# Optimization experiments

Measured on AMD Instinct MI355X. Metric: run time of the kernel, lower is better.

Reference implementation:

```python
import jax, jax.numpy as jnp
import numpy as np

B, C_IN, T, N_VERTEX = 2, 64, 12, 2048
KS, C_OUT = 3, 64
NNZ = 98304  # Ks * n_vertex * avg_degree(16)


def setup_inputs() -> dict:
    key = jax.random.key(0)
    k0, k1, k2, k3, k4, k5 = jax.random.split(key, 6)
    x = jax.random.normal(k0, (B, C_IN, T, N_VERTEX), jnp.float32)
    # kaiming-uniform-ish init for weight [Ks, c_in, c_out]
    bound_w = float(np.sqrt(6.0 / C_IN))
    weight = jax.random.uniform(k1, (KS, C_IN, C_OUT), jnp.float32, -bound_w, bound_w)
    bound_b = float(1.0 / np.sqrt(C_OUT))
    bias = jax.random.uniform(k2, (C_OUT,), jnp.float32, -bound_b, bound_b)
    # sparse chebconv_filter in COO: shape [n_vertex, Ks*n_vertex]
    filter_rows = jax.random.randint(k3, (NNZ,), 0, N_VERTEX)
    filter_cols = jax.random.randint(k4, (NNZ,), 0, KS * N_VERTEX)
    filter_vals = jax.random.normal(k5, (NNZ,), jnp.float32) * 0.1
    return dict(x=x, weight=weight, bias=bias, filter_vals=filter_vals,
                filter_rows=filter_rows, filter_cols=filter_cols)


def reference(x, weight, bias, filter_vals, filter_rows, filter_cols):
    b, c_in, t, n = x.shape
    ks, _, c_out = weight.shape
    # dense GEMM: [B*T*n (row-major flatten of B,c_in,T,n keeping last dim c_in), c_in] @ [c_in, Ks*c_out]
    xw = x.reshape(-1, c_in) @ weight.reshape(c_in, ks * c_out)  # [B*c_in*T*n/c_in, Ks*c_out]
    xw = xw.reshape(n * ks, -1)                                  # [n*Ks, B*T*c_out]
    # spmm with COO filter [n, n*Ks]: gather columns, scale, scatter-add to rows
    gathered = filter_vals[:, None] * xw[filter_cols]            # [nnz, B*T*c_out]
    y = jax.ops.segment_sum(gathered, filter_rows, num_segments=N_VERTEX)  # [n, B*T*c_out]
    return y.reshape(-1, c_out) + bias                           # [n*B*T, c_out]
```

## Files before the change

kernel.cpp:

```cpp
#include <hip/hip_runtime.h>
#include <hip/hip_bf16.h>

#define NV      2048
#define NNZ_    98304
#define KDIM    64
#define WCOLS   192
#define ZROWS   16384
#define BUCKET  128

typedef __attribute__((ext_vector_type(8))) short  short8;
typedef __attribute__((ext_vector_type(8))) unsigned short ushort8;
typedef __attribute__((ext_vector_type(4))) float  float4v;

__device__ __forceinline__ float b2f(unsigned short h) {
    return __uint_as_float(((unsigned int)h) << 16);
}
__device__ __forceinline__ unsigned short f2b(float f) {
    return __bfloat16_as_ushort(__float2bfloat16(f));
}

__global__ __launch_bounds__(256) void scatter_kernel(
    const int4* __restrict__ rows4, const int4* __restrict__ cols4,
    const float4* __restrict__ vals4, const float* __restrict__ wf,
    int* __restrict__ cnt, int2* __restrict__ sedge,
    unsigned short* __restrict__ wt)
{
    if (blockIdx.x == NNZ_ / 1024) {
        for (int i = 0; i < 48; i++) {
            const int e = threadIdx.x + 256 * i;
            const int k = e / WCOLS, n = e - k * WCOLS;
            wt[n * KDIM + k] = f2b(wf[e]);
        }
        return;
    }
    const int t = blockIdx.x * 256 + threadIdx.x;
    const int4   r = rows4[t];
    const int4   c = cols4[t];
    const float4 v = vals4[t];
    int p;
    p = atomicAdd(&cnt[r.x], 1); if (p < BUCKET) sedge[r.x * BUCKET + p] = make_int2(c.x * 512, __float_as_int(v.x));
    p = atomicAdd(&cnt[r.y], 1); if (p < BUCKET) sedge[r.y * BUCKET + p] = make_int2(c.y * 512, __float_as_int(v.y));
    p = atomicAdd(&cnt[r.z], 1); if (p < BUCKET) sedge[r.z * BUCKET + p] = make_int2(c.z * 512, __float_as_int(v.z));
    p = atomicAdd(&cnt[r.w], 1); if (p < BUCKET) sedge[r.w * BUCKET + p] = make_int2(c.w * 512, __float_as_int(v.w));
}

__global__ __launch_bounds__(256) void spmmx_kernel(
    const float* __restrict__ xf,
    const int* __restrict__ cnt,
    const int2* __restrict__ sedge,
    unsigned short* __restrict__ zb)
{
    __shared__ int2 se_lds[4][64];
    const int b    = blockIdx.x;
    const int g    = b & 7;
    const int w    = threadIdx.x >> 6;
    const int row  = (b >> 3) * 4 + w;
    const int lane = threadIdx.x & 63;

    int n = cnt[row];
    if (n > BUCKET) n = BUCKET;
    const int2* se = sedge + row * BUCKET;
    const int off = g * KDIM + lane;

    float acc = 0.f;
    for (int base = 0; base < n; base += 64) {
        const int m = (n - base < 64) ? (n - base) : 64;
        const int li = (lane < m) ? (base + lane) : (base + m - 1);
        se_lds[w][lane] = se[li];

        int i = 0;
        for (; i + 16 <= m; i += 16) {
            int2 e[16];
#pragma unroll
            for (int u = 0; u < 16; u++) e[u] = se_lds[w][i + u];
            float x[16];
#pragma unroll
            for (int u = 0; u < 16; u++) x[u] = xf[e[u].x + off];
#pragma unroll
            for (int u = 0; u < 16; u++) acc += __int_as_float(e[u].y) * x[u];
        }
        for (; i + 8 <= m; i += 8) {
            const int2 e0 = se_lds[w][i    ], e1 = se_lds[w][i + 1];
            const int2 e2 = se_lds[w][i + 2], e3 = se_lds[w][i + 3];
            const int2 e4 = se_lds[w][i + 4], e5 = se_lds[w][i + 5];
            const int2 e6 = se_lds[w][i + 6], e7 = se_lds[w][i + 7];
            const float x0 = xf[e0.x + off], x1 = xf[e1.x + off];
            const float x2 = xf[e2.x + off], x3 = xf[e3.x + off];
            const float x4 = xf[e4.x + off], x5 = xf[e5.x + off];
            const float x6 = xf[e6.x + off], x7 = xf[e7.x + off];
            acc += __int_as_float(e0.y) * x0 + __int_as_float(e1.y) * x1
                 + __int_as_float(e2.y) * x2 + __int_as_float(e3.y) * x3
                 + __int_as_float(e4.y) * x4 + __int_as_float(e5.y) * x5
                 + __int_as_float(e6.y) * x6 + __int_as_float(e7.y) * x7;
        }
        for (; i < m; i++) {
            const int2 e = se_lds[w][i];
            acc += __int_as_float(e.y) * xf[e.x + off];
        }
    }
    zb[(size_t)(row * 8 + g) * KDIM + lane] = f2b(acc);
}

__global__ __launch_bounds__(256) void gemm2_kernel(
    const unsigned short* __restrict__ zb, const unsigned short* __restrict__ wt,
    const float* __restrict__ bias, float* __restrict__ out)
{
    __shared__ unsigned short Wt[WCOLS * 72];
    __shared__ unsigned short Zs[64 * 72];
    const int tid = threadIdx.x;
    const int m0  = blockIdx.x * 64;

#pragma unroll
    for (int u = 0; u < 2; u++) {
        const int ch = tid + 256 * u;
        const ushort8 p = *(const ushort8*)(zb + (size_t)m0 * KDIM + ch * 8);
        const int row = ch >> 3, col = (ch & 7) * 8;
        *(ushort8*)&Zs[row * 72 + col] = p;
    }
#pragma unroll
    for (int u = 0; u < 6; u++) {
        const int ch = tid + 256 * u;
        const ushort8 p = *(const ushort8*)(wt + ch * 8);
        const int row = ch >> 3, col = (ch & 7) * 8;
        *(ushort8*)&Wt[row * 72 + col] = p;
    }
    __syncthreads();

    const int lane = tid & 63;
    const int mt   = tid >> 6;
    const int q    = lane >> 4;
    const int c    = lane & 15;

    const short8 a0 = *(const short8*)&Zs[(mt * 16 + c) * 72 + q * 8];
    const short8 a1 = *(const short8*)&Zs[(mt * 16 + c) * 72 + 32 + q * 8];

    float4v acc[12];
#pragma unroll
    for (int nt = 0; nt < 12; nt++) {
        const short8 b0 = *(const short8*)&Wt[(nt * 16 + c) * 72 + q * 8];
        const short8 b1 = *(const short8*)&Wt[(nt * 16 + c) * 72 + 32 + q * 8];
        float4v d = {0.f, 0.f, 0.f, 0.f};
        d = __builtin_amdgcn_mfma_f32_16x16x32_bf16(a0, b0, d, 0, 0, 0);
        d = __builtin_amdgcn_mfma_f32_16x16x32_bf16(a1, b1, d, 0, 0, 0);
        acc[nt] = d;
    }

    const int rbase = m0 + mt * 16 + q * 4;
#pragma unroll
    for (int nt = 0; nt < 12; nt++) {
        const int col = nt * 16 + c;
        const float bb = bias[col & 63];
#pragma unroll
        for (int r = 0; r < 4; r++)
            out[(size_t)(rbase + r) * WCOLS + col] = acc[nt][r] + bb;
    }
}

extern "C" void kernel_launch(void* const* d_in, const int* in_sizes, int n_in,
                              void* d_out, int out_size, void* d_ws, size_t ws_size,
                              hipStream_t stream) {
    const float* x    = (const float*)d_in[0];
    const float* wgt  = (const float*)d_in[1];
    const float* bias = (const float*)d_in[2];
    const float* fval = (const float*)d_in[3];
    const int* frow   = (const int*)d_in[4];
    const int* fcol   = (const int*)d_in[5];

    int* cnt = (int*)d_ws;
    int2* sedge = (int2*)(cnt + 2048);
    unsigned short* wt = (unsigned short*)(sedge + NV * BUCKET);
    unsigned short* zb = wt + 12288;

    hipMemsetAsync(cnt, 0, 2048 * sizeof(int), stream);
    scatter_kernel<<<NNZ_ / 1024 + 1, 256, 0, stream>>>(
        (const int4*)frow, (const int4*)fcol, (const float4*)fval, wgt,
        cnt, sedge, wt);
    spmmx_kernel <<<ZROWS / 4, 256, 0, stream>>>(x, cnt, sedge, zb);
    gemm2_kernel <<<ZROWS / 64, 256, 0, stream>>>(zb, wt, bias, (float*)d_out);
}
```

Before: 109.0 us.

## Convert x to fp16 in scatter pass and gather 4-wide in SpMM

Adds extra blocks to the scatter kernel that convert the fp32 input x into an fp16 copy in workspace. The SpMM kernel then gathers 8-byte fp16 chunks, with each lane covering four channels and four lane groups handling different edges. Partial sums are combined with cross-lane shuffles. This halves gather bytes and cuts the number of load instructions, at the cost of an extra full pass over x and reduced input precision.

```diff
diff --git a/kernel.cpp b/kernel.cpp
--- a/kernel.cpp
+++ b/kernel.cpp
@@ -1,5 +1,6 @@
 #include <hip/hip_runtime.h>
 #include <hip/hip_bf16.h>
+#include <hip/hip_fp16.h>
 
 #define NV      2048
 #define NNZ_    98304
@@ -7,25 +8,52 @@
 #define WCOLS   192
 #define ZROWS   16384
 #define BUCKET  128
+#define XELEMS  (3 * NV * 512)
+#define CONVB   768
 
 typedef __attribute__((ext_vector_type(8))) short  short8;
 typedef __attribute__((ext_vector_type(8))) unsigned short ushort8;
 typedef __attribute__((ext_vector_type(4))) float  float4v;
 
-__device__ __forceinline__ float b2f(unsigned short h) {
-    return __uint_as_float(((unsigned int)h) << 16);
-}
 __device__ __forceinline__ unsigned short f2b(float f) {
     return __bfloat16_as_ushort(__float2bfloat16(f));
+}
+__device__ __forceinline__ unsigned int f2h2(float a, float b) {
+    return (unsigned int)__half_as_ushort(__float2half(a)) |
+           ((unsigned int)__half_as_ushort(__float2half(b)) << 16);
+}
+__device__ __forceinline__ float2 h2f2(unsigned int u) {
+    const __half2 h = *reinterpret_cast<const __half2*>(&u);
+    return __half22float2(h);
 }
 
 __global__ __launch_bounds__(256) void scatter_kernel(
     const int4* __restrict__ rows4, const int4* __restrict__ cols4,
     const float4* __restrict__ vals4, const float* __restrict__ wf,
+    const float* __restrict__ xf,
     int* __restrict__ cnt, int2* __restrict__ sedge,
-    unsigned short* __restrict__ wt)
+    unsigned short* __restrict__ wt, unsigned short* __restrict__ xh)
 {
-    if (blockIdx.x == NNZ_ / 1024) {
+    const int bb = blockIdx.x;
+    if (bb > NNZ_ / 1024) {
+        const int cb = bb - (NNZ_ / 1024 + 1);
+        const size_t base = ((size_t)cb * 256 + threadIdx.x) * 16;
+        const float4* xin = (const float4*)(xf + base);
+        float4 f[4];
+#pragma unroll
+        for (int u = 0; u < 4; u++) f[u] = xin[u];
+        unsigned int p[8];
+#pragma unroll
+        for (int u = 0; u < 4; u++) {
+            p[2 * u]     = f2h2(f[u].x, f[u].y);
+            p[2 * u + 1] = f2h2(f[u].z, f[u].w);
+        }
+        uint4* xo = (uint4*)(xh + base);
+        xo[0] = make_uint4(p[0], p[1], p[2], p[3]);
+        xo[1] = make_uint4(p[4], p[5], p[6], p[7]);
+        return;
+    }
+    if (bb == NNZ_ / 1024) {
         for (int i = 0; i < 48; i++) {
             const int e = threadIdx.x + 256 * i;
             const int k = e / WCOLS, n = e - k * WCOLS;
@@ -33,7 +61,7 @@
         }
         return;
     }
-    const int t = blockIdx.x * 256 + threadIdx.x;
+    const int t = bb * 256 + threadIdx.x;
     const int4   r = rows4[t];
     const int4   c = cols4[t];
     const float4 v = vals4[t];
@@ -45,7 +73,7 @@
 }
 
 __global__ __launch_bounds__(256) void spmmx_kernel(
-    const float* __restrict__ xf,
+    const unsigned short* __restrict__ xh,
     const int* __restrict__ cnt,
     const int2* __restrict__ sedge,
     unsigned short* __restrict__ zb)
@@ -56,49 +84,71 @@
     const int w    = threadIdx.x >> 6;
     const int row  = (b >> 3) * 4 + w;
     const int lane = threadIdx.x & 63;
+    const int grp  = lane >> 4;
+    const int l    = lane & 15;
 
     int n = cnt[row];
     if (n > BUCKET) n = BUCKET;
     const int2* se = sedge + row * BUCKET;
-    const int off = g * KDIM + lane;
-
-    float acc = 0.f;
+    const int off = g * KDIM + l * 4;
+
+    float a0 = 0.f, a1 = 0.f, a2 = 0.f, a3 = 0.f;
     for (int base = 0; base < n; base += 64) {
         const int m = (n - base < 64) ? (n - base) : 64;
         const int li = (lane < m) ? (base + lane) : (base + m - 1);
         se_lds[w][lane] = se[li];
 
         int i = 0;
+        for (; i + 32 <= m; i += 32) {
+            int2 e[8];
+#pragma unroll
+            for (int u = 0; u < 8; u++) e[u] = se_lds[w][i + u * 4 + grp];
+            uint2 xb[8];
+#pragma unroll
+            for (int u = 0; u < 8; u++) xb[u] = *(const uint2*)(xh + e[u].x + off);
+#pragma unroll
+            for (int u = 0; u < 8; u++) {
+                const float v = __int_as_float(e[u].y);
+                const float2 x01 = h2f2(xb[u].x), x23 = h2f2(xb[u].y);
+                a0 += v * x01.x; a1 += v * x01.y;
+                a2 += v * x23.x; a3 += v * x23.y;
+            }
+        }
         for (; i + 16 <= m; i += 16) {
-            int2 e[16];
-#pragma unroll
-            for (int u = 0; u < 16; u++) e[u] = se_lds[w][i + u];
-            float x[16];
-#pragma unroll
-            for (int u = 0; u < 16; u++) x[u] = xf[e[u].x + off];
-#pragma unroll
-            for (int u = 0; u < 16; u++) acc += __int_as_float(e[u].y) * x[u];
-        }
-        for (; i + 8 <= m; i += 8) {
-            const int2 e0 = se_lds[w][i    ], e1 = se_lds[w][i + 1];
-            const int2 e2 = se_lds[w][i + 2], e3 = se_lds[w][i + 3];
-            const int2 e4 = se_lds[w][i + 4], e5 = se_lds[w][i + 5];
-            const int2 e6 = se_lds[w][i + 6], e7 = se_lds[w][i + 7];
-            const float x0 = xf[e0.x + off], x1 = xf[e1.x + off];
-            const float x2 = xf[e2.x + off], x3 = xf[e3.x + off];
-            const float x4 = xf[e4.x + off], x5 = xf[e5.x + off];
-            const float x6 = xf[e6.x + off], x7 = xf[e7.x + off];
-            acc += __int_as_float(e0.y) * x0 + __int_as_float(e1.y) * x1
-                 + __int_as_float(e2.y) * x2 + __int_as_float(e3.y) * x3
-                 + __int_as_float(e4.y) * x4 + __int_as_float(e5.y) * x5
-                 + __int_as_float(e6.y) * x6 + __int_as_float(e7.y) * x7;
-        }
-        for (; i < m; i++) {
-            const int2 e = se_lds[w][i];
-            acc += __int_as_float(e.y) * xf[e.x + off];
-        }
-    }
-    zb[(size_t)(row * 8 + g) * KDIM + lane] = f2b(acc);
+            int2 e[4];
+#pragma unroll
+            for (int u = 0; u < 4; u++) e[u] = se_lds[w][i + u * 4 + grp];
+            uint2 xb[4];
+#pragma unroll
+            for (int u = 0; u < 4; u++) xb[u] = *(const uint2*)(xh + e[u].x + off);
+#pragma unroll
+            for (int u = 0; u < 4; u++) {
+                const float v = __int_as_float(e[u].y);
+                const float2 x01 = h2f2(xb[u].x), x23 = h2f2(xb[u].y);
+                a0 += v * x01.x; a1 += v * x01.y;
+                a2 += v * x23.x; a3 += v * x23.y;
+            }
+        }
+        for (; i < m; i += 4) {
+            const int j  = (i + grp < m) ? (i + grp) : (m - 1);
+            const int2 e = se_lds[w][j];
+            const float v = (i + grp < m) ? __int_as_float(e.y) : 0.f;
+            const uint2 xb = *(const uint2*)(xh + e.x + off);
+            const float2 x01 = h2f2(xb.x), x23 = h2f2(xb.y);
+            a0 += v * x01.x; a1 += v * x01.y;
+            a2 += v * x23.x; a3 += v * x23.y;
+        }
+    }
+    a0 += __shfl_xor(a0, 16); a1 += __shfl_xor(a1, 16);
+    a2 += __shfl_xor(a2, 16); a3 += __shfl_xor(a3, 16);
+    a0 += __shfl_xor(a0, 32); a1 += __shfl_xor(a1, 32);
+    a2 += __shfl_xor(a2, 32); a3 += __shfl_xor(a3, 32);
+    if (grp == 0) {
+        uint2 o;
+        o.x = (unsigned)f2b(a0) | ((unsigned)f2b(a1) << 16);
+        o.y = (unsigned)f2b(a2) | ((unsigned)f2b(a3) << 16);
+        *(uint2*)(zb + (size_t)(row * 8 + g) * KDIM + l * 4) = o;
+    }
 }
 
 __global__ __launch_bounds__(256) void gemm2_kernel(
@@ -170,11 +220,12 @@
     int2* sedge = (int2*)(cnt + 2048);
     unsigned short* wt = (unsigned short*)(sedge + NV * BUCKET);
     unsigned short* zb = wt + 12288;
+    unsigned short* xh = zb + (size_t)ZROWS * KDIM;
 
     hipMemsetAsync(cnt, 0, 2048 * sizeof(int), stream);
-    scatter_kernel<<<NNZ_ / 1024 + 1, 256, 0, stream>>>(
-        (const int4*)frow, (const int4*)fcol, (const float4*)fval, wgt,
-        cnt, sedge, wt);
-    spmmx_kernel <<<ZROWS / 4, 256, 0, stream>>>(x, cnt, sedge, zb);
+    scatter_kernel<<<NNZ_ / 1024 + 1 + CONVB, 256, 0, stream>>>(
+        (const int4*)frow, (const int4*)fcol, (const float4*)fval, wgt, x,
+        cnt, sedge, wt, xh);
+    spmmx_kernel <<<ZROWS / 4, 256, 0, stream>>>(xh, cnt, sedge, zb);
     gemm2_kernel <<<ZROWS / 64, 256, 0, stream>>>(zb, wt, bias, (float*)d_out);
 }
```

Result: no change. 109.1 us (+0.1%).
